# Performance work log

Hardware: AMD Instinct MI355X
Metric: run time of the kernel (lower is better)

Reference implementation:

```python
import jax, jax.numpy as jnp
import numpy as np

DIM = 2048
ORDER = 1
# upper-triangular index pairs (i<j), row-major over i then j — matches torch loop order
_IU_ROWS, _IU_COLS = np.triu_indices(DIM, k=1)


def setup_inputs() -> dict:
    key = jax.random.key(0)
    k1, k2 = jax.random.split(key)
    num_params = DIM * (DIM - 1) // 2
    x = jax.random.normal(k1, (4, 4096, DIM), dtype=jnp.float32)
    angles = jax.random.normal(k2, (num_params,), dtype=jnp.float32) * 0.01
    bias = jnp.zeros((DIM,), dtype=jnp.float32)
    return {"x": x, "angles": angles, "bias": bias}


def _skew_symmetric(angles):
    # A[i,j] = angles[k], A[j,i] = -angles[k] for upper-tri (i<j)
    A = jnp.zeros((DIM, DIM), dtype=angles.dtype)
    A = A.at[_IU_ROWS, _IU_COLS].set(angles)
    return A - A.T


def _cayley_approx(A, order=ORDER):
    # W = (I + A + ... + A^order) @ (I + A)
    I = jnp.eye(DIM, dtype=A.dtype)
    inv_approx = I
    A_power = A
    for _ in range(order):
        inv_approx = inv_approx + A_power
        A_power = A_power @ A
    return inv_approx @ (I + A)


def reference(x, angles, bias):
    A = _skew_symmetric(angles)
    W = _cayley_approx(A)
    # [b, s, d] @ [d, d] -> [b, s, d]
    out = jnp.einsum('bsd,de->bse', x, W) + bias
    return out
```

## Files before the change

### kernel.cpp

```cpp
#include <hip/hip_runtime.h>
#include <stdint.h>

#define DIM 2048

typedef short short8 __attribute__((ext_vector_type(8)));
typedef float f32x4 __attribute__((ext_vector_type(4)));

__device__ __forceinline__ unsigned short f2bf(float f) {
    union { float f; unsigned int u; } v;
    v.f = f;
    unsigned int r = v.u + 0x7FFFu + ((v.u >> 16) & 1u);
    return (unsigned short)(r >> 16);
}
__device__ __forceinline__ float bf2f(unsigned short u) {
    union { unsigned int u; float f; } v;
    v.u = ((unsigned int)u) << 16;
    return v.f;
}

__device__ __forceinline__ void async16(const unsigned short* g, unsigned short* l) {
    __builtin_amdgcn_global_load_lds(
        (__attribute__((address_space(1))) void*)(uintptr_t)g,
        (__attribute__((address_space(3))) void*)(uintptr_t)l,
        16, 0, 0);
}

__global__ __launch_bounds__(256) void build_A_tiled(const float* __restrict__ ang,
                                                     unsigned short* __restrict__ A) {
    __shared__ float tile[64][65];
    int b = blockIdx.x;
    int ti = 0, rem = b;
    while (rem >= 32 - ti) { rem -= 32 - ti; ++ti; }
    const int tj = ti + rem;
    const int t  = threadIdx.x;
    const int lj = t & 63;
    const int lw = t >> 6;
    const bool diag = (ti == tj);

#pragma unroll
    for (int m = 0; m < 16; ++m) {
        const int li = lw * 16 + m;
        const int i = ti * 64 + li;
        const int j = tj * 64 + lj;
        float v = 0.0f;
        if (i < j) v = ang[i * (4095 - i) / 2 + (j - i - 1)];
        tile[li][lj] = v;
    }
    __syncthreads();

#pragma unroll
    for (int m = 0; m < 16; ++m) {
        const int li = lw * 16 + m;
        float v;
        if (diag) {
            if (li < lj)      v =  tile[li][lj];
            else if (li > lj) v = -tile[lj][li];
            else              v = 0.0f;
        } else {
            v = tile[li][lj];
        }
        A[(size_t)(ti * 64 + li) * DIM + tj * 64 + lj] = f2bf(v);
    }
    if (!diag) {
#pragma unroll
        for (int m = 0; m < 16; ++m) {
            const int li = lw * 16 + m;
            A[(size_t)(tj * 64 + li) * DIM + ti * 64 + lj] = f2bf(-tile[lj][li]);
        }
    }
}

__global__ void cvt_f32_bf16(const float* __restrict__ in, unsigned short* __restrict__ out) {
    int i = (blockIdx.x * 256 + threadIdx.x) * 4;
    const float4 v = *(const float4*)(in + i);
    ushort4 o;
    o.x = f2bf(v.x); o.y = f2bf(v.y); o.z = f2bf(v.z); o.w = f2bf(v.w);
    *(ushort4*)(out + i) = o;
}

__global__ __launch_bounds__(256) void gemm_s64(
        const unsigned short* __restrict__ A,
        unsigned short* __restrict__ Wt) {
    __shared__ __align__(16) unsigned short ldsA[64 * 64];
    __shared__ __align__(16) unsigned short ldsB[64 * 64];
    const int K = DIM, N = DIM;

    const int t    = threadIdx.x;
    const int bn   = blockIdx.x * 64;
    const int bm   = blockIdx.y * 64;
    const int lane = t & 63;
    const int wave = t >> 6;
    const int waveM = (wave >> 1) * 32;
    const int waveN = (wave & 1) * 32;
    const int fm = lane & 15;
    const int fq = lane >> 4;

    f32x4 acc[2][2];
#pragma unroll
    for (int i = 0; i < 2; ++i)
#pragma unroll
        for (int j = 0; j < 2; ++j)
            acc[i][j] = (f32x4){0.f, 0.f, 0.f, 0.f};

    const int trow   = t >> 3;
    const int tchunk = (t & 7) ^ (trow & 7);
    const unsigned short* gA = A + (size_t)(bm + trow) * K + tchunk * 8;
    const unsigned short* gB = A + (size_t)(bn + trow) * K + tchunk * 8;
    const size_t rowskip = (size_t)32 * K;
    unsigned short* lA = ldsA + t * 8;
    unsigned short* lB = ldsB + t * 8;

    for (int kt = 0; kt < K; kt += 64) {
        __syncthreads();
        async16(gA + kt, lA);
        async16(gA + kt + rowskip, lA + 2048);
        async16(gB + kt, lB);
        async16(gB + kt + rowskip, lB + 2048);
        __syncthreads();

#pragma unroll
        for (int ks = 0; ks < 2; ++ks) {
            short8 af[2], bfv[2];
#pragma unroll
            for (int i = 0; i < 2; ++i) {
                const int rowA = waveM + i * 16 + fm;
                const int rowB = waveN + i * 16 + fm;
                af[i]  = *(const short8*)(ldsA + rowA * 64 + (((ks << 2) + fq) ^ (rowA & 7)) * 8);
                bfv[i] = *(const short8*)(ldsB + rowB * 64 + (((ks << 2) + fq) ^ (rowB & 7)) * 8);
            }
#pragma unroll
            for (int i = 0; i < 2; ++i)
#pragma unroll
                for (int j = 0; j < 2; ++j)
                    acc[i][j] = __builtin_amdgcn_mfma_f32_16x16x32_bf16(
                        af[i], bfv[j], acc[i][j], 0, 0, 0);
        }
    }

#pragma unroll
    for (int i = 0; i < 2; ++i) {
#pragma unroll
        for (int j = 0; j < 2; ++j) {
            const int col = bn + waveN + j * 16 + fm;
#pragma unroll
            for (int r = 0; r < 4; ++r) {
                const int row = bm + waveM + i * 16 + fq * 4 + r;
                const float a = bf2f(A[(size_t)row * N + col]);
                const float w = (row == col ? 1.0f : 0.0f) - 2.0f * a - acc[i][j][r];
                Wt[(size_t)row * N + col] = f2bf(w);
            }
        }
    }
}


#define WAITV(N) asm volatile("s_waitcnt vmcnt(" #N ")" ::: "memory")
#define BAR() do { asm volatile("" ::: "memory"); __builtin_amdgcn_s_barrier(); asm volatile("" ::: "memory"); } while (0)

#define STG_A(BUF, R0, KT) async16(gA + (size_t)(R0) * 2048 + (KT), &ldsA[BUF][(R0) * 64 + t * 8])
#define STG_B(BUF, R0, KT) async16(gB + (size_t)(R0) * 2048 + (KT), &ldsB[BUF][(R0) * 64 + t * 8])

#define READ_A(BUF, IH) do { \
    _Pragma("unroll") \
    for (int ii = 0; ii < 4; ++ii) { \
        const int row  = waveM + (IH) * 64 + ii * 16 + fm; \
        const int base = row * 64; \
        af[ii][0] = *(const short8*)(&ldsA[BUF][base + ((fq    ) ^ (row & 7)) * 8]); \
        af[ii][1] = *(const short8*)(&ldsA[BUF][base + ((fq + 4) ^ (row & 7)) * 8]); \
    } } while (0)

#define READ_B(BUF, JH) do { \
    _Pragma("unroll") \
    for (int jj = 0; jj < 2; ++jj) { \
        const int row  = (JH) * 128 + wn * 32 + jj * 16 + fm; \
        const int base = row * 64; \
        bfr[JH][jj][0] = *(const short8*)(&ldsB[BUF][base + ((fq    ) ^ (row & 7)) * 8]); \
        bfr[JH][jj][1] = *(const short8*)(&ldsB[BUF][base + ((fq + 4) ^ (row & 7)) * 8]); \
    } } while (0)

#define MMAQ(IH, JH) do { \
    __builtin_amdgcn_s_setprio(1); \
    _Pragma("unroll") \
    for (int ks = 0; ks < 2; ++ks) \
    _Pragma("unroll") \
    for (int ii = 0; ii < 4; ++ii) \
    _Pragma("unroll") \
    for (int jj = 0; jj < 2; ++jj) \
        acc[(IH) * 4 + ii][(JH) * 2 + jj] = __builtin_amdgcn_mfma_f32_16x16x32_bf16( \
            af[ii][ks], bfr[JH][jj][ks], acc[(IH) * 4 + ii][(JH) * 2 + jj], 0, 0, 0); \
    __builtin_amdgcn_s_setprio(0); \
} while (0)

#define KTILE(BUF, KTN, PRE, VN) do { \
    WAITV(VN); \
    BAR(); \
     \
    READ_A(BUF, 0); \
    READ_B(BUF, 0); \
    MMAQ(0, 0); \
    BAR(); \
     \
    if (PRE) { STG_A(BUF, 0, KTN); STG_A(BUF, 128, KTN); } \
    READ_B(BUF, 1); \
    MMAQ(0, 1); \
    BAR(); \
     \
    if (PRE) { STG_B(BUF, 0, KTN); STG_B(BUF, 64, KTN); } \
    READ_A(BUF, 1); \
    MMAQ(1, 0); \
    BAR(); \
     \
    if (PRE) { STG_B(BUF, 128, KTN); STG_B(BUF, 192, KTN); STG_A(BUF, 64, KTN); STG_A(BUF, 192, KTN); } \
    MMAQ(1, 1); \
    BAR(); \
} while (0)

__global__ __launch_bounds__(512, 2) void gemm_main(
        const unsigned short* __restrict__ Aop,
        const unsigned short* __restrict__ Bop,
        int M, int N, int K,
        const float* __restrict__ bias,
        float* __restrict__ out) {
    __shared__ __align__(16) unsigned short ldsA[2][256 * 64];
    __shared__ __align__(16) unsigned short ldsB[2][256 * 64];

    const int t    = threadIdx.x;
    const int bn   = blockIdx.x * 256;
    const int bm   = blockIdx.y * 256;
    const int lane = t & 63;
    const int wave = t >> 6;
    const int wm   = wave >> 2;
    const int wn   = wave & 3;
    const int waveM = wm * 128;
    const int fm = lane & 15;
    const int fq = lane >> 4;

    f32x4 acc[8][4];
#pragma unroll
    for (int i = 0; i < 8; ++i)
#pragma unroll
        for (int j = 0; j < 4; ++j)
            acc[i][j] = (f32x4){0.f, 0.f, 0.f, 0.f};

    short8 af[4][2];
    short8 bfr[2][2][2];

    const int trow   = t >> 3;
    const int tchunk = (t & 7) ^ (trow & 7);
    const unsigned short* gA = Aop + (size_t)(bm + trow) * 2048 + tchunk * 8;
    const unsigned short* gB = Bop + (size_t)(bn + trow) * 2048 + tchunk * 8;

    STG_A(0, 0, 0);   STG_A(0, 128, 0);  STG_B(0, 0, 0);   STG_B(0, 64, 0);
    STG_B(0, 128, 0); STG_B(0, 192, 0);  STG_A(0, 64, 0);  STG_A(0, 192, 0);
    STG_A(1, 0, 64);  STG_A(1, 128, 64); STG_B(1, 0, 64);  STG_B(1, 64, 64);
    STG_B(1, 128, 64);STG_B(1, 192, 64); STG_A(1, 64, 64); STG_A(1, 192, 64);

#pragma unroll 1
    for (int it = 0; it < 15; ++it) {
        const int kt = it * 128;
        KTILE(0, kt + 128, true, 8);
        KTILE(1, kt + 192, true, 8);
    }
    KTILE(0, 0, false, 8);
    KTILE(1, 0, false, 0);

#pragma unroll
    for (int i = 0; i < 8; ++i) {
        const int row0 = bm + waveM + i * 16 + fq * 4;
#pragma unroll
        for (int j = 0; j < 4; ++j) {
            const int col = bn + (j >> 1) * 128 + wn * 32 + (j & 1) * 16 + fm;
            const float b = bias[col];
#pragma unroll
            for (int r = 0; r < 4; ++r)
                out[(size_t)(row0 + r) * 2048 + col] = acc[i][j][r] + b;
        }
    }
}

extern "C" void kernel_launch(void* const* d_in, const int* in_sizes, int n_in,
                              void* d_out, int out_size, void* d_ws, size_t ws_size,
                              hipStream_t stream) {
    const float* x      = (const float*)d_in[0];
    const float* angles = (const float*)d_in[1];
    const float* bias   = (const float*)d_in[2];
    float* out = (float*)d_out;

    char* ws = (char*)d_ws;
    unsigned short* Abf = (unsigned short*)ws;
    unsigned short* Wt  = (unsigned short*)(ws + (8u << 20));
    unsigned short* xbf = (unsigned short*)(ws + (16u << 20));

    const int M = 4 * 4096;
    const int n_elem_x = M * DIM;

    build_A_tiled<<<528, 256, 0, stream>>>(angles, Abf);
    cvt_f32_bf16<<<(n_elem_x / 4) / 256, 256, 0, stream>>>(x, xbf);

    gemm_s64<<<dim3(DIM / 64, DIM / 64), 256, 0, stream>>>(Abf, Wt);

    gemm_main<<<dim3(DIM / 256, M / 256), 512, 0, stream>>>(
        xbf, Wt, M, DIM, DIM, bias, out);
}
```

Measured before the change: 376.8 us.

## Software-pipeline LDS fragment reads across k-tiles and swizzle block order

Reorders the main GEMM k-tile loop so fragment reads from shared memory for the next quarter and next tile are issued after each MFMA group, overlapping LDS reads with matrix math and dropping one barrier per tile. Prefetch stores are redistributed and the vmcnt wait is relaxed. Both GEMM kernels also remap block indices with a swizzle to improve L2 locality. The new schedule risks LDS read/write hazards if barrier placement is wrong, and adds register pressure.

```diff
diff --git a/kernel.cpp b/kernel.cpp
--- a/kernel.cpp
+++ b/kernel.cpp
@@ -86,8 +86,10 @@
     const int K = DIM, N = DIM;
 
     const int t    = threadIdx.x;
-    const int bn   = blockIdx.x * 64;
-    const int bm   = blockIdx.y * 64;
+    const int flat = blockIdx.y * 32 + blockIdx.x;
+    const int swz  = (flat & 7) * 128 + (flat >> 3);
+    const int bn   = (swz & 31) * 64;
+    const int bm   = (swz >> 5) * 64;
     const int lane = t & 63;
     const int wave = t >> 6;
     const int waveM = (wave >> 1) * 32;
@@ -160,7 +162,7 @@
 #define STG_A(BUF, R0, KT) async16(gA + (size_t)(R0) * 2048 + (KT), &ldsA[BUF][(R0) * 64 + t * 8])
 #define STG_B(BUF, R0, KT) async16(gB + (size_t)(R0) * 2048 + (KT), &ldsB[BUF][(R0) * 64 + t * 8])
 
-#define READ_A(BUF, IH) do { \
+#define READ_A_(BUF, IH) do { \
     _Pragma("unroll") \
     for (int ii = 0; ii < 4; ++ii) { \
         const int row  = waveM + (IH) * 64 + ii * 16 + fm; \
@@ -169,7 +171,7 @@
         af[ii][1] = *(const short8*)(&ldsA[BUF][base + ((fq + 4) ^ (row & 7)) * 8]); \
     } } while (0)
 
-#define READ_B(BUF, JH) do { \
+#define READ_B_(BUF, JH) do { \
     _Pragma("unroll") \
     for (int jj = 0; jj < 2; ++jj) { \
         const int row  = (JH) * 128 + wn * 32 + jj * 16 + fm; \
@@ -191,28 +193,34 @@
     __builtin_amdgcn_s_setprio(0); \
 } while (0)
 
-#define KTILE(BUF, KTN, PRE, VN) do { \
+#define TILE(BUF, KTN, PRE, VN, NXT) do { \
+     \
+    BAR(); \
+    if (PRE) { STG_A(BUF, 0, KTN); STG_A(BUF, 128, KTN); STG_B(BUF, 0, KTN); STG_B(BUF, 64, KTN); } \
+    MMAQ(0, 0); \
+    READ_B_(BUF, 1); \
+     \
+    BAR(); \
+    if (PRE) { STG_B(BUF, 128, KTN); STG_B(BUF, 192, KTN); } \
+    MMAQ(0, 1); \
+    READ_A_(BUF, 1); \
+     \
     WAITV(VN); \
     BAR(); \
+    if (PRE) { STG_A(BUF, 64, KTN); STG_A(BUF, 192, KTN); } \
+    MMAQ(1, 0); \
+    if (NXT) READ_B_((BUF) ^ 1, 0); \
      \
-    READ_A(BUF, 0); \
-    READ_B(BUF, 0); \
-    MMAQ(0, 0); \
     BAR(); \
-     \
-    if (PRE) { STG_A(BUF, 0, KTN); STG_A(BUF, 128, KTN); } \
-    READ_B(BUF, 1); \
-    MMAQ(0, 1); \
-    BAR(); \
-     \
-    if (PRE) { STG_B(BUF, 0, KTN); STG_B(BUF, 64, KTN); } \
-    READ_A(BUF, 1); \
-    MMAQ(1, 0); \
-    BAR(); \
-     \
-    if (PRE) { STG_B(BUF, 128, KTN); STG_B(BUF, 192, KTN); STG_A(BUF, 64, KTN); STG_A(BUF, 192, KTN); } \
     MMAQ(1, 1); \
-    BAR(); \
+    if (NXT) READ_A_((BUF) ^ 1, 0); \
+} while (0)
+
+#define TILE_LAST(BUF) do { \
+    BAR(); MMAQ(0, 0); READ_B_(BUF, 1); \
+    BAR(); MMAQ(0, 1); READ_A_(BUF, 1); \
+    BAR(); MMAQ(1, 0); \
+    MMAQ(1, 1); \
 } while (0)
 
 __global__ __launch_bounds__(512, 2) void gemm_main(
@@ -225,8 +233,10 @@
     __shared__ __align__(16) unsigned short ldsB[2][256 * 64];
 
     const int t    = threadIdx.x;
-    const int bn   = blockIdx.x * 256;
-    const int bm   = blockIdx.y * 256;
+    const int flat = blockIdx.y * 8 + blockIdx.x;
+    const int swz  = (flat & 7) * 64 + (flat >> 3);
+    const int bn   = (swz & 7) * 256;
+    const int bm   = (swz >> 3) * 256;
     const int lane = t & 63;
     const int wave = t >> 6;
     const int wm   = wave >> 2;
@@ -254,15 +264,19 @@
     STG_B(0, 128, 0); STG_B(0, 192, 0);  STG_A(0, 64, 0);  STG_A(0, 192, 0);
     STG_A(1, 0, 64);  STG_A(1, 128, 64); STG_B(1, 0, 64);  STG_B(1, 64, 64);
     STG_B(1, 128, 64);STG_B(1, 192, 64); STG_A(1, 64, 64); STG_A(1, 192, 64);
+    WAITV(8);
+    BAR();
+    READ_A_(0, 0);
+    READ_B_(0, 0);
 
 #pragma unroll 1
     for (int it = 0; it < 15; ++it) {
         const int kt = it * 128;
-        KTILE(0, kt + 128, true, 8);
-        KTILE(1, kt + 192, true, 8);
-    }
-    KTILE(0, 0, false, 8);
-    KTILE(1, 0, false, 0);
+        TILE(0, kt + 128, 1, 6, 1);
+        TILE(1, kt + 192, 1, 6, 1);
+    }
+    TILE(0, 0, 0, 0, 1);
+    TILE_LAST(1);
 
 #pragma unroll
     for (int i = 0; i < 8; ++i) {
```

New measurement: 371.3 us. Within noise of the previous version (-1.5%).
